# Optimization experiments

Measured on AMD Instinct MI355X. Metric: run time of the kernel, lower is better.

The kernel has to match this reference:

```python
import jax, jax.numpy as jnp
import numpy as np
from jax import lax

NF = 64
KS = 3
PAD = 1
TOPK = 2
DG = 8          # deformable_groups
N = KS * KS     # 9 sampling points


def conv3x3(x, w, b):
    y = lax.conv_general_dilated(x, w, (1, 1), 'SAME',
                                 dimension_numbers=('NCHW', 'OIHW', 'NCHW'))
    return y + b[None, :, None, None]


def lrelu(x):
    return jnp.where(x >= 0, x, 0.1 * x)


def dsp_sample(x, feat, w_om, b_om):
    """Modulated deformable sampling (DSP_sep2): returns the N bilinearly
    sampled, mask-modulated taps per pixel, shape (B, C, N, H, W)."""
    B, C, H, W = x.shape
    Cg = C // DG
    om = conv3x3(feat, w_om, b_om)              # (B, 3*DG*N, H, W)
    o1, o2, m = jnp.split(om, 3, axis=1)
    off_y = o1.reshape(B, DG, N, H, W)
    off_x = o2.reshape(B, DG, N, H, W)
    mask = jax.nn.sigmoid(m).reshape(B, DG, 1, N, H * W)
    kk = (jnp.arange(KS) - PAD).astype(jnp.float32)
    kdy = jnp.repeat(kk, KS)                    # (N,) kernel row offsets
    kdx = jnp.tile(kk, KS)                      # (N,) kernel col offsets
    ii = jnp.arange(H, dtype=jnp.float32)
    jj = jnp.arange(W, dtype=jnp.float32)
    ys = ii[None, None, None, :, None] + kdy[None, None, :, None, None] + off_y
    xs = jj[None, None, None, None, :] + kdx[None, None, :, None, None] + off_x
    y0 = jnp.floor(ys)
    x0 = jnp.floor(xs)
    xf = x.reshape(B, DG, Cg, H * W)
    out = jnp.zeros((B, DG, Cg, N, H * W), x.dtype)
    # bilinear interpolation with zero padding outside the image
    for dy in (0.0, 1.0):
        for dx in (0.0, 1.0):
            yi = y0 + dy
            xi = x0 + dx
            wgt = (1.0 - jnp.abs(ys - yi)) * (1.0 - jnp.abs(xs - xi))
            valid = (yi >= 0) & (yi <= H - 1) & (xi >= 0) & (xi <= W - 1)
            lin = (jnp.clip(yi, 0, H - 1) * W + jnp.clip(xi, 0, W - 1)).astype(jnp.int32)
            g = jnp.take_along_axis(xf[:, :, :, None, :],
                                    lin.reshape(B, DG, 1, N, H * W), axis=-1)
            out = out + g * jnp.where(valid, wgt, 0.0).reshape(B, DG, 1, N, H * W)
    return (out * mask).reshape(B, C, N, H, W)


def setup_inputs() -> dict:
    key = jax.random.key(0)
    ks = jax.random.split(key, 9)
    B, C, H, W = 2, NF, 192, 192

    def rn(k, s, sc=1.0):
        return jax.random.normal(k, s, jnp.float32) * sc

    return {
        'query': rn(ks[0], (B, C, H, W)),
        'key':   rn(ks[1], (B, C, H, W)),
        'value': rn(ks[2], (B, C, H, W)),
        'w1': rn(ks[3], (C, 2 * C, 3, 3), 0.05), 'b1': rn(ks[4], (C,), 0.05),
        'w2': rn(ks[5], (C, C, 3, 3), 0.05),     'b2': rn(ks[6], (C,), 0.05),
        'w_om': rn(ks[7], (3 * DG * N, C, 3, 3), 0.01),
        'b_om': rn(ks[8], (3 * DG * N,), 0.01),
    }


def reference(query, key, value, w1, b1, w2, b2, w_om, b_om):
    B, C, H, W = query.shape
    HW = H * W
    feat = lrelu(conv3x3(jnp.concatenate([query, key], axis=1), w1, b1))
    feat = lrelu(conv3x3(feat, w2, b2))
    # deformable sampled keys: (B, C, N, H, W) -> (B, HW, N, C)
    key_off = dsp_sample(key, feat, w_om, b_om).transpose(0, 3, 4, 2, 1).reshape(B, HW, N, C)
    q = query.reshape(B, C, HW).transpose(0, 2, 1)            # (B, HW, C)
    rel = jnp.einsum('bpnc,bpc->bpn', key_off, q)             # relevance scores
    topv, topi = lax.top_k(rel, TOPK)                         # (B, HW, TOPK)
    corr = jax.nn.softmax(topv, axis=-1)
    val_off = dsp_sample(value, feat, w_om, b_om).transpose(0, 3, 4, 2, 1).reshape(B, HW, N, C)
    k_sel = jnp.take_along_axis(key_off, topi[..., None], axis=2)  # (B, HW, TOPK, C)
    v_sel = jnp.take_along_axis(val_off, topi[..., None], axis=2)
    k_upd = jnp.einsum('bptc,bpt->bpc', k_sel, corr)
    v_out = jnp.einsum('bptc,bpt->bpc', v_sel, corr).transpose(0, 2, 1)  # (B, C, HW)
    weight = jnp.einsum('bpc,bpc->bp', q, k_upd)              # (B, HW)
    return (weight, v_out)
```

## Files before the change

kernel.cpp:

```cpp
#include <hip/hip_runtime.h>
#include <math.h>

#define H_  192
#define W_  192
#define HW_ (192 * 192)
#define B_  2
#define C_  64

typedef __attribute__((ext_vector_type(8))) short short8;
typedef __attribute__((ext_vector_type(4))) short short4v;
typedef __attribute__((ext_vector_type(4))) float float4v;
typedef _Float16 __attribute__((ext_vector_type(8))) half8;

union hbits { _Float16 f; short s; };
__device__ __forceinline__ void split2(float x, short& h, short& l) {
    _Float16 hf = (_Float16)x;
    float r = (x - (float)hf) * 4096.f;
    _Float16 lf = (_Float16)r;
    hbits u;
    u.f = hf; h = u.s;
    u.f = lf; l = u.s;
}

__device__ __forceinline__ float bilin_dot(const float* __restrict__ pl,
                                           float ys, float xs, int c4,
                                           float4v q4) {
    float y0 = floorf(ys), x0 = floorf(xs);
    float fy = ys - y0, fx = xs - x0;
    int iy = (int)y0, ix = (int)x0;
    float acc = 0.f;
    #pragma unroll
    for (int dy = 0; dy < 2; ++dy) {
        #pragma unroll
        for (int dx = 0; dx < 2; ++dx) {
            int yy = iy + dy, xx = ix + dx;
            float wgt = (dy ? fy : 1.f - fy) * (dx ? fx : 1.f - fx);
            bool valid = (yy >= 0) && (yy < H_) && (xx >= 0) && (xx < W_);
            int yc = min(max(yy, 0), H_ - 1);
            int xc = min(max(xx, 0), W_ - 1);
            const float4v v = *(const float4v*)(pl + (size_t)(yc * W_ + xc) * 64 + c4);
            float d = v[0] * q4[0] + v[1] * q4[1] + v[2] * q4[2] + v[3] * q4[3];
            acc += valid ? wgt * d : 0.f;
        }
    }
    return acc;
}
__device__ __forceinline__ float4v bilin_v4(const float* __restrict__ pl,
                                            float ys, float xs, int c4) {
    float y0 = floorf(ys), x0 = floorf(xs);
    float fy = ys - y0, fx = xs - x0;
    int iy = (int)y0, ix = (int)x0;
    float4v acc;
    acc[0] = acc[1] = acc[2] = acc[3] = 0.f;
    #pragma unroll
    for (int dy = 0; dy < 2; ++dy) {
        #pragma unroll
        for (int dx = 0; dx < 2; ++dx) {
            int yy = iy + dy, xx = ix + dx;
            float wgt = (dy ? fy : 1.f - fy) * (dx ? fx : 1.f - fx);
            bool valid = (yy >= 0) && (yy < H_) && (xx >= 0) && (xx < W_);
            float wz = valid ? wgt : 0.f;
            int yc = min(max(yy, 0), H_ - 1);
            int xc = min(max(xx, 0), W_ - 1);
            const float4v v = *(const float4v*)(pl + (size_t)(yc * W_ + xc) * 64 + c4);
            #pragma unroll
            for (int r = 0; r < 4; ++r) acc[r] += wz * v[r];
        }
    }
    return acc;
}

__global__ __launch_bounds__(256) void prep_w_k(
    const float* __restrict__ w1, const float* __restrict__ w2,
    const float* __restrict__ wom,
    short* __restrict__ pw1, short* __restrict__ pw2, short* __restrict__ pwom)
{
    int idx = blockIdx.x * 256 + threadIdx.x;
    int arr;
    if (idx < 144 * 512) { arr = 0; }
    else if (idx < (144 + 72) * 512) { arr = 1; idx -= 144 * 512; }
    else if (idx < (144 + 72 + 252) * 512) { arr = 2; idx -= (144 + 72) * 512; }
    else return;
    int frag = idx >> 9, within = idx & 511;
    int lane = within >> 3, j = within & 7;
    int KS   = (arr == 0) ? 4 : 2;
    int mt   = frag / (9 * KS);
    int rem  = frag % (9 * KS);
    int kk   = rem / KS;
    int s    = rem % KS;
    int co   = mt * 16 + (lane & 15);
    int c    = s * 32 + (lane >> 4) * 8 + j;
    float v = 0.f;
    if (arr == 0)      v = w1[(co * 128 + c) * 9 + kk];
    else if (arr == 1) v = w2[(co * 64 + c) * 9 + kk];
    else if (co < 216) v = wom[(co * 64 + c) * 9 + kk];
    short h, l;
    split2(v, h, l);
    short* dst = (arr == 0) ? pw1 : (arr == 1) ? pw2 : pwom;
    size_t base = (size_t)frag * 1024 + lane * 8 + j;
    dst[base]       = h;
    dst[base + 512] = l;
}

__global__ __launch_bounds__(256) void nchw_to_nhwc(
    const float* __restrict__ key, const float* __restrict__ value,
    float* __restrict__ kT, float* __restrict__ vT)
{
    __shared__ float sm[64][65];
    const int tid = threadIdx.x;
    const int p0  = blockIdx.x * 64;
    const int b   = blockIdx.y;
    const float* src = blockIdx.z ? value : key;
    float*       dst = blockIdx.z ? vT    : kT;
    const int pp = tid & 63;
    const int r0 = tid >> 6;
    #pragma unroll
    for (int c = r0; c < 64; c += 4)
        sm[c][pp] = src[(size_t)(b * 64 + c) * HW_ + p0 + pp];
    __syncthreads();
    const int cc = tid & 63;
    #pragma unroll
    for (int pw = r0; pw < 64; pw += 4)
        dst[((size_t)b * HW_ + p0 + pw) * 64 + cc] = sm[cc][pw];
}

template<int CIN, int MT, bool LRELU, int OUTMODE, bool FROMF32>
__global__ __launch_bounds__(256) void conv_mfma(
    const void* __restrict__ in0v, const void* __restrict__ in1v,
    const short* __restrict__ pw, const float* __restrict__ bias,
    void* __restrict__ outv)
{
    constexpr int KS   = CIN / 32;
    constexpr int MTW  = MT / 2;
    constexpr int LSTR = 72;
    __shared__ __align__(16) short smem[66 * LSTR];

    const int tid  = threadIdx.x;
    const int lane = tid & 63;
    const int w    = tid >> 6;
    const int wh   = w & 1;
    const int wn   = w >> 1;
    const int quad = lane >> 4;
    const int nn   = lane & 15;

    const int flat = blockIdx.x;
    const int xcd  = flat & 7;
    const int cc_  = flat >> 3;
    const int b    = xcd >> 2;
    const int r4   = xcd & 3;
    const int i    = r4 * 48 + cc_ / 3;
    const int j0   = (cc_ % 3) * 64;
    const int mt0  = wh * MTW;

    constexpr float CSC = 1.f / 4096.f;

    float4v accM[MTW][2];
    #pragma unroll
    for (int m = 0; m < MTW; ++m)
        #pragma unroll
        for (int t = 0; t < 2; ++t)
            #pragma unroll
            for (int r = 0; r < 4; ++r) accM[m][t][r] = 0.f;

    float4v zvec;
    zvec[0] = zvec[1] = zvec[2] = zvec[3] = 0.f;

    for (int ky = 0; ky < 3; ++ky) {
        const int row = i + ky - 1;
        const bool rowok = (row >= 0) && (row < H_);
        for (int s = 0; s < KS; ++s) {
            __syncthreads();
            if (FROMF32) {
                const float* src = (s < KS / 2) ? (const float*)in0v
                                                : (const float*)in1v;
                const int cbase = (s & (KS / 2 - 1)) * 32;
                for (int idx = tid; idx < 32 * 66; idx += 256) {
                    int ci = idx / 66, px = idx - ci * 66;
                    int col = j0 - 1 + px;
                    float v = 0.f;
                    if (rowok && col >= 0 && col < W_)
                        v = src[(size_t)(b * 64 + cbase + ci) * HW_ + row * W_ + col];
                    short h, l;
                    split2(v, h, l);
                    smem[px * LSTR + ci]      = h;
                    smem[px * LSTR + 32 + ci] = l;
                }
            } else {
                const short* src = (const short*)in0v
                                 + (size_t)b * HW_ * (2 * CIN);
                for (int idx = tid; idx < 66 * 16; idx += 256) {
                    int px = idx >> 4, r = idx & 15;
                    int limb = r >> 3, dq = r & 7;
                    int col = j0 - 1 + px;
                    unsigned long long v = 0;
                    if (rowok && col >= 0 && col < W_)
                        v = *(const unsigned long long*)(src
                              + (size_t)(row * W_ + col) * (2 * CIN)
                              + limb * CIN + s * 32 + dq * 4);
                    *(unsigned long long*)(&smem[px * LSTR + limb * 32 + dq * 4]) = v;
                }
            }
            __syncthreads();

            #pragma unroll
            for (int kx = 0; kx < 3; ++kx) {
                const int kk = ky * 3 + kx;
                half8 bh[2], bl[2];
                #pragma unroll
                for (int t2 = 0; t2 < 2; ++t2) {
                    const int t = wn * 2 + t2;
                    const short* bp = &smem[(t * 16 + nn + kx) * LSTR + quad * 8];
                    bh[t2] = *(const half8*)bp;
                    bl[t2] = *(const half8*)(bp + 32);
                }
                #pragma unroll
                for (int m = 0; m < MTW; ++m) {
                    const short* ap = pw
                        + ((size_t)(((mt0 + m) * 9 + kk) * KS + s)) * 1024
                        + lane * 8;
                    half8 ah = *(const half8*)ap;
                    half8 al = *(const half8*)(ap + 512);
                    float4v t0, t1;
                    accM[m][0] = __builtin_amdgcn_mfma_f32_16x16x32_f16(ah, bh[0], accM[m][0], 0, 0, 0);
                    t0         = __builtin_amdgcn_mfma_f32_16x16x32_f16(ah, bl[0], zvec,       0, 0, 0);
                    accM[m][1] = __builtin_amdgcn_mfma_f32_16x16x32_f16(ah, bh[1], accM[m][1], 0, 0, 0);
                    t1         = __builtin_amdgcn_mfma_f32_16x16x32_f16(ah, bl[1], zvec,       0, 0, 0);
                    t0         = __builtin_amdgcn_mfma_f32_16x16x32_f16(al, bh[0], t0,         0, 0, 0);
                    t1         = __builtin_amdgcn_mfma_f32_16x16x32_f16(al, bh[1], t1,         0, 0, 0);
                    #pragma unroll
                    for (int r = 0; r < 4; ++r) {
                        accM[m][0][r] += t0[r] * CSC;
                        accM[m][1][r] += t1[r] * CSC;
                    }
                }
            }
        }
    }

    #pragma unroll
    for (int m = 0; m < MTW; ++m) {
        const int co0 = (mt0 + m) * 16 + quad * 4;
        #pragma unroll
        for (int t2 = 0; t2 < 2; ++t2) {
            const int t = wn * 2 + t2;
            const int p = i * W_ + j0 + t * 16 + nn;
            if (OUTMODE == 0) {
                short* feat = (short*)outv;
                short4v hv, lv;
                #pragma unroll
                for (int r = 0; r < 4; ++r) {
                    float x = accM[m][t2][r] + bias[co0 + r];
                    if (LRELU) x = (x >= 0.f) ? x : 0.1f * x;
                    short h, l;
                    split2(x, h, l);
                    hv[r] = h; lv[r] = l;
                }
                short* dp = feat + ((size_t)b * HW_ + p) * 128 + co0;
                *(short4v*)dp        = hv;
                *(short4v*)(dp + 64) = lv;
            } else {
                if (co0 < 216) {
                    float* om = (float*)outv;
                    float4v v;
                    #pragma unroll
                    for (int r = 0; r < 4; ++r)
                        v[r] = accM[m][t2][r] + bias[co0 + r];
                    *(float4v*)(om + ((size_t)b * HW_ + p) * 216 + co0) = v;
                }
            }
        }
    }
}

__global__ __launch_bounds__(256) void sampler_k(
    const float* __restrict__ query, const float* __restrict__ kT,
    const float* __restrict__ vT, const float* __restrict__ om,
    float* __restrict__ out_w, float* __restrict__ out_v)
{
    __shared__ float sq[16 * 68];
    const int tid  = threadIdx.x;
    const int bb   = blockIdx.x;
    const int b    = bb / 2304;
    const int pblk = (bb - b * 2304) * 16;

    #pragma unroll
    for (int k = 0; k < 4; ++k) {
        int idx = tid + k * 256;
        int c   = idx >> 4;
        int px  = idx & 15;
        sq[px * 68 + c] = query[(size_t)(b * 64 + c) * HW_ + pblk + px];
    }
    __syncthreads();

    const int lane   = tid & 63;
    const int w      = tid >> 6;
    const int px_sub = lane >> 4;
    const int cl     = lane & 15;
    const int c4     = cl * 4;
    const int g      = cl >> 1;
    const int p      = pblk + w * 4 + px_sub;
    const int i      = p / W_;
    const int j      = p - i * W_;

    const float4v q4 = *(const float4v*)&sq[(w * 4 + px_sub) * 68 + c4];

    const float* omb = om + ((size_t)b * HW_ + p) * 216;
    float offy[9], offx[9], mk[9];
    #pragma unroll
    for (int n = 0; n < 9; ++n) {
        offy[n] = omb[g * 9 + n];
        offx[n] = omb[72 + g * 9 + n];
        float mv = omb[144 + g * 9 + n];
        mk[n] = 1.f / (1.f + expf(-mv));
    }

    const float* kpl = kT + (size_t)b * HW_ * 64;
    float rel[9];
    #pragma unroll
    for (int n = 0; n < 9; ++n) {
        float ys = (float)i + (float)(n / 3 - 1) + offy[n];
        float xs = (float)j + (float)(n % 3 - 1) + offx[n];
        float d = bilin_dot(kpl, ys, xs, c4, q4) * mk[n];
        #pragma unroll
        for (int off = 1; off < 16; off <<= 1)
            d += __shfl_xor(d, off, 64);
        rel[n] = d;
    }

    int n0 = 0; float v0 = rel[0];
    #pragma unroll
    for (int n = 1; n < 9; ++n) { if (rel[n] > v0) { v0 = rel[n]; n0 = n; } }
    int n1 = -1; float v1 = -1e30f;
    #pragma unroll
    for (int n = 0; n < 9; ++n) { if (n != n0 && rel[n] > v1) { v1 = rel[n]; n1 = n; } }

    float e1  = expf(v1 - v0);
    float inv = 1.f / (1.f + e1);
    float c0 = inv, c1 = e1 * inv;

    if (cl == 0) out_w[(size_t)b * HW_ + p] = c0 * v0 + c1 * v1;

    float oy0 = 0, ox0 = 0, m0 = 0, oy1 = 0, ox1 = 0, m1 = 0;
    #pragma unroll
    for (int n = 0; n < 9; ++n) {
        if (n == n0) { oy0 = offy[n]; ox0 = offx[n]; m0 = mk[n]; }
        if (n == n1) { oy1 = offy[n]; ox1 = offx[n]; m1 = mk[n]; }
    }

    const float* vpl = vT + (size_t)b * HW_ * 64;
    float ys0 = (float)i + (float)(n0 / 3 - 1) + oy0;
    float xs0 = (float)j + (float)(n0 % 3 - 1) + ox0;
    float ys1 = (float)i + (float)(n1 / 3 - 1) + oy1;
    float xs1 = (float)j + (float)(n1 % 3 - 1) + ox1;
    float4v vv0 = bilin_v4(vpl, ys0, xs0, c4);
    float4v vv1 = bilin_v4(vpl, ys1, xs1, c4);
    float w0 = c0 * m0, w1s = c1 * m1;
    #pragma unroll
    for (int r = 0; r < 4; ++r)
        out_v[(size_t)(b * C_ + c4 + r) * HW_ + p] = w0 * vv0[r] + w1s * vv1[r];
}

extern "C" void kernel_launch(void* const* d_in, const int* in_sizes, int n_in,
                              void* d_out, int out_size, void* d_ws, size_t ws_size,
                              hipStream_t stream)
{
    const float* query = (const float*)d_in[0];
    const float* key   = (const float*)d_in[1];
    const float* value = (const float*)d_in[2];
    const float* w1    = (const float*)d_in[3];
    const float* b1    = (const float*)d_in[4];
    const float* w2    = (const float*)d_in[5];
    const float* b2    = (const float*)d_in[6];
    const float* wom   = (const float*)d_in[7];
    const float* bom   = (const float*)d_in[8];
    float* out = (float*)d_out;

    char* ws = (char*)d_ws;
    short* f1  = (short*)(ws);
    float* om  = (float*)(ws);
    short* f2  = (short*)(ws + 63700992);
    float* kT  = (float*)(ws + 63700992);
    float* vT  = (float*)(ws + 82575360);
    short* pwom= (short*)(ws + 92012544);
    short* pw1 = (short*)(ws + 92786688);
    short* pw2 = (short*)(ws + 93229056);

    prep_w_k<<<936, 256, 0, stream>>>(w1, w2, wom, pw1, pw2, pwom);

    conv_mfma<128, 4,  true,  0, true ><<<1152, 256, 0, stream>>>(query, key, pw1, b1, (void*)f1);
    conv_mfma<64,  4,  true,  0, false><<<1152, 256, 0, stream>>>(f1, nullptr, pw2, b2, (void*)f2);
    conv_mfma<64,  14, false, 1, false><<<1152, 256, 0, stream>>>(f2, nullptr, pwom, bom, (void*)om);

    nchw_to_nhwc<<<dim3(576, B_, 2), 256, 0, stream>>>(key, value, kT, vT);

    float* out_w = out;
    float* out_v = out + (size_t)B_ * HW_;
    sampler_k<<<(B_ * HW_) / 16, 256, 0, stream>>>(query, kT, vT, om, out_w, out_v);
}
```

Before: 429.8 us.

## Stage all input channels per kernel row in LDS with XOR swizzle

The conv kernel now loads every input-channel slice for a kernel row into shared memory in one pass, instead of one 32-channel slice at a time. This cuts the number of barriers and load phases from KS per row to one. For the fp32-input variant it adds an XOR swizzle on the LDS column index to reduce bank conflicts, and the hi/lo-split variant loads contiguous 8-byte chunks. The cost is a much larger LDS footprint (up to about 37KB), which may lower occupancy.

```diff
diff --git a/kernel.cpp b/kernel.cpp
--- a/kernel.cpp
+++ b/kernel.cpp
@@ -132,7 +132,7 @@
 {
     constexpr int KS   = CIN / 32;
     constexpr int MTW  = MT / 2;
-    constexpr int LSTR = 72;
+    constexpr int LSTR = FROMF32 ? 280 : 136;
     __shared__ __align__(16) short smem[66 * LSTR];
 
     const int tid  = threadIdx.x;
@@ -168,50 +168,58 @@
     for (int ky = 0; ky < 3; ++ky) {
         const int row = i + ky - 1;
         const bool rowok = (row >= 0) && (row < H_);
-        for (int s = 0; s < KS; ++s) {
-            __syncthreads();
-            if (FROMF32) {
-                const float* src = (s < KS / 2) ? (const float*)in0v
-                                                : (const float*)in1v;
-                const int cbase = (s & (KS / 2 - 1)) * 32;
-                for (int idx = tid; idx < 32 * 66; idx += 256) {
-                    int ci = idx / 66, px = idx - ci * 66;
-                    int col = j0 - 1 + px;
-                    float v = 0.f;
-                    if (rowok && col >= 0 && col < W_)
-                        v = src[(size_t)(b * 64 + cbase + ci) * HW_ + row * W_ + col];
-                    short h, l;
-                    split2(v, h, l);
-                    smem[px * LSTR + ci]      = h;
-                    smem[px * LSTR + 32 + ci] = l;
+        __syncthreads();
+        if (FROMF32) {
+            for (int idx = tid; idx < 128 * 66; idx += 256) {
+                int ci = idx / 66, px = idx - ci * 66;
+                int col = j0 - 1 + px;
+                float v = 0.f;
+                if (rowok && col >= 0 && col < W_) {
+                    const float* src = (ci < 64) ? (const float*)in0v
+                                                 : (const float*)in1v;
+                    v = src[(size_t)(b * 64 + (ci & 63)) * HW_ + row * W_ + col];
                 }
-            } else {
-                const short* src = (const short*)in0v
-                                 + (size_t)b * HW_ * (2 * CIN);
-                for (int idx = tid; idx < 66 * 16; idx += 256) {
-                    int px = idx >> 4, r = idx & 15;
-                    int limb = r >> 3, dq = r & 7;
-                    int col = j0 - 1 + px;
-                    unsigned long long v = 0;
-                    if (rowok && col >= 0 && col < W_)
-                        v = *(const unsigned long long*)(src
-                              + (size_t)(row * W_ + col) * (2 * CIN)
-                              + limb * CIN + s * 32 + dq * 4);
-                    *(unsigned long long*)(&smem[px * LSTR + limb * 32 + dq * 4]) = v;
-                }
+                short h, l;
+                split2(v, h, l);
+                int s   = ci >> 5;
+                int c5  = ci & 31;
+                int msk = ((px >> 3) & 7) << 3;
+                short* rp = &smem[px * LSTR];
+                rp[(s * 64 + c5) ^ msk]      = h;
+                rp[(s * 64 + 32 + c5) ^ msk] = l;
             }
-            __syncthreads();
-
+        } else {
+            const short* srcb = (const short*)in0v + (size_t)b * HW_ * (2 * CIN);
+            for (int idx = tid; idx < 66 * (CIN / 2); idx += 256) {
+                int px = idx / (CIN / 2), r = idx - px * (CIN / 2);
+                int col = j0 - 1 + px;
+                unsigned long long v = 0;
+                if (rowok && col >= 0 && col < W_)
+                    v = *(const unsigned long long*)(srcb
+                          + (size_t)(row * W_ + col) * (2 * CIN) + r * 4);
+                *(unsigned long long*)(&smem[px * LSTR + r * 4]) = v;
+            }
+        }
+        __syncthreads();
+
+        #pragma unroll
+        for (int kx = 0; kx < 3; ++kx) {
+            const int kk = ky * 3 + kx;
             #pragma unroll
-            for (int kx = 0; kx < 3; ++kx) {
-                const int kk = ky * 3 + kx;
+            for (int s = 0; s < KS; ++s) {
                 half8 bh[2], bl[2];
                 #pragma unroll
                 for (int t2 = 0; t2 < 2; ++t2) {
-                    const int t = wn * 2 + t2;
-                    const short* bp = &smem[(t * 16 + nn + kx) * LSTR + quad * 8];
-                    bh[t2] = *(const half8*)bp;
-                    bl[t2] = *(const half8*)(bp + 32);
+                    const int rr = (wn * 2 + t2) * 16 + nn + kx;
+                    const short* rp = &smem[rr * LSTR];
+                    if (FROMF32) {
+                        const int msk = ((rr >> 3) & 7) << 3;
+                        bh[t2] = *(const half8*)&rp[(s * 64 + quad * 8) ^ msk];
+                        bl[t2] = *(const half8*)&rp[(s * 64 + 32 + quad * 8) ^ msk];
+                    } else {
+                        bh[t2] = *(const half8*)&rp[s * 32 + quad * 8];
+                        bl[t2] = *(const half8*)&rp[CIN + s * 32 + quad * 8];
+                    }
                 }
                 #pragma unroll
                 for (int m = 0; m < MTW; ++m) {
```

Measured after the change: 438.1 us. No clear change (+1.9%).

## Pre-pad inputs into split-fp16 NHWC and read conv operands directly from global

Applied to the files above, without the earlier changes.

Adds a pack kernel that converts query/key into a zero-padded NHWC hi/lo fp16 buffer, and makes the intermediate feature maps padded with zeroed borders. The conv kernels then drop the LDS staging, the barriers and the per-pixel boundary checks, and load MFMA B operands straight from global memory. In exchange there are extra kernels and padded buffers, and the same input pixels are loaded repeatedly from global/L2 rather than once per block into shared memory. The workspace offsets are also rearranged, so buffers that share memory need checking.

```diff
diff --git a/kernel.cpp b/kernel.cpp
--- a/kernel.cpp
+++ b/kernel.cpp
@@ -6,6 +6,7 @@
 #define HW_ (192 * 192)
 #define B_  2
 #define C_  64
+#define PW_ 194
 
 typedef __attribute__((ext_vector_type(8))) short short8;
 typedef __attribute__((ext_vector_type(4))) short short4v;
@@ -102,6 +103,49 @@
     dst[base + 512] = l;
 }
 
+__global__ __launch_bounds__(256) void pack_qk(
+    const float* __restrict__ q, const float* __restrict__ k,
+    short* __restrict__ qk2)
+{
+    const int prow = blockIdx.x;
+    const int b    = blockIdx.y;
+    const int row  = prow - 1;
+    const bool rok = (row >= 0) && (row < H_);
+    short* dst = qk2 + ((size_t)(b * PW_ + prow) * PW_) * 256;
+    for (int idx = threadIdx.x; idx < 128 * PW_; idx += 256) {
+        int ci = idx / PW_, pcol = idx - ci * PW_;
+        int col = pcol - 1;
+        float v = 0.f;
+        if (rok && col >= 0 && col < W_) {
+            const float* src = (ci < 64) ? q : k;
+            v = src[(size_t)(b * 64 + (ci & 63)) * HW_ + row * W_ + col];
+        }
+        short h, l;
+        split2(v, h, l);
+        dst[(size_t)pcol * 256 + ci]       = h;
+        dst[(size_t)pcol * 256 + 128 + ci] = l;
+    }
+}
+
+__global__ __launch_bounds__(256) void zero_borders(
+    short* __restrict__ f1p, short* __restrict__ f2p)
+{
+    const int prow = blockIdx.x;
+    const int b    = blockIdx.y;
+    short* dst = (blockIdx.z ? f2p : f1p) + ((size_t)(b * PW_ + prow) * PW_) * 128;
+    if (prow == 0 || prow == PW_ - 1) {
+        for (int idx = threadIdx.x; idx < PW_ * 128; idx += 256) dst[idx] = 0;
+    } else {
+        for (int idx = threadIdx.x; idx < 256; idx += 256) {
+            dst[idx] = 0;
+            dst[(size_t)(PW_ - 1) * 128 + idx - 128 * (idx >> 7)] = 0;
+        }
+        int t = threadIdx.x;
+        if (t < 128) dst[t] = 0;
+        else dst[(size_t)(PW_ - 1) * 128 + (t - 128)] = 0;
+    }
+}
+
 __global__ __launch_bounds__(256) void nchw_to_nhwc(
     const float* __restrict__ key, const float* __restrict__ value,
     float* __restrict__ kT, float* __restrict__ vT)
@@ -124,16 +168,13 @@
         dst[((size_t)b * HW_ + p0 + pw) * 64 + cc] = sm[cc][pw];
 }
 
-template<int CIN, int MT, bool LRELU, int OUTMODE, bool FROMF32>
-__global__ __launch_bounds__(256) void conv_mfma(
-    const void* __restrict__ in0v, const void* __restrict__ in1v,
-    const short* __restrict__ pw, const float* __restrict__ bias,
-    void* __restrict__ outv)
-{
-    constexpr int KS   = CIN / 32;
-    constexpr int MTW  = MT / 2;
-    constexpr int LSTR = 72;
-    __shared__ __align__(16) short smem[66 * LSTR];
+template<int CIN, int MT, bool LRELU, int OUTMODE>
+__global__ __launch_bounds__(256) void conv_direct(
+    const short* __restrict__ in, const short* __restrict__ pw,
+    const float* __restrict__ bias, void* __restrict__ outv)
+{
+    constexpr int KS  = CIN / 32;
+    constexpr int MTW = MT / 2;
 
     const int tid  = threadIdx.x;
     const int lane = tid & 63;
@@ -166,52 +207,20 @@
     zvec[0] = zvec[1] = zvec[2] = zvec[3] = 0.f;
 
     for (int ky = 0; ky < 3; ++ky) {
-        const int row = i + ky - 1;
-        const bool rowok = (row >= 0) && (row < H_);
-        for (int s = 0; s < KS; ++s) {
-            __syncthreads();
-            if (FROMF32) {
-                const float* src = (s < KS / 2) ? (const float*)in0v
-                                                : (const float*)in1v;
-                const int cbase = (s & (KS / 2 - 1)) * 32;
-                for (int idx = tid; idx < 32 * 66; idx += 256) {
-                    int ci = idx / 66, px = idx - ci * 66;
-                    int col = j0 - 1 + px;
-                    float v = 0.f;
-                    if (rowok && col >= 0 && col < W_)
-                        v = src[(size_t)(b * 64 + cbase + ci) * HW_ + row * W_ + col];
-                    short h, l;
-                    split2(v, h, l);
-                    smem[px * LSTR + ci]      = h;
-                    smem[px * LSTR + 32 + ci] = l;
-                }
-            } else {
-                const short* src = (const short*)in0v
-                                 + (size_t)b * HW_ * (2 * CIN);
-                for (int idx = tid; idx < 66 * 16; idx += 256) {
-                    int px = idx >> 4, r = idx & 15;
-                    int limb = r >> 3, dq = r & 7;
-                    int col = j0 - 1 + px;
-                    unsigned long long v = 0;
-                    if (rowok && col >= 0 && col < W_)
-                        v = *(const unsigned long long*)(src
-                              + (size_t)(row * W_ + col) * (2 * CIN)
-                              + limb * CIN + s * 32 + dq * 4);
-                    *(unsigned long long*)(&smem[px * LSTR + limb * 32 + dq * 4]) = v;
-                }
-            }
-            __syncthreads();
-
+        const short* rowp = in + ((size_t)(b * PW_ + (i + ky)) * PW_) * (2 * CIN);
+        #pragma unroll
+        for (int kx = 0; kx < 3; ++kx) {
+            const int kk = ky * 3 + kx;
             #pragma unroll
-            for (int kx = 0; kx < 3; ++kx) {
-                const int kk = ky * 3 + kx;
+            for (int s = 0; s < KS; ++s) {
                 half8 bh[2], bl[2];
                 #pragma unroll
                 for (int t2 = 0; t2 < 2; ++t2) {
-                    const int t = wn * 2 + t2;
-                    const short* bp = &smem[(t * 16 + nn + kx) * LSTR + quad * 8];
+                    const int pcol = j0 + kx + (wn * 2 + t2) * 16 + nn;
+                    const short* bp = rowp + (size_t)pcol * (2 * CIN)
+                                    + s * 32 + quad * 8;
                     bh[t2] = *(const half8*)bp;
-                    bl[t2] = *(const half8*)(bp + 32);
+                    bl[t2] = *(const half8*)(bp + CIN);
                 }
                 #pragma unroll
                 for (int m = 0; m < MTW; ++m) {
@@ -243,8 +252,9 @@
         #pragma unroll
         for (int t2 = 0; t2 < 2; ++t2) {
             const int t = wn * 2 + t2;
-            const int p = i * W_ + j0 + t * 16 + nn;
             if (OUTMODE == 0) {
+                const size_t pp = ((size_t)(b * PW_ + i + 1) * PW_
+                                   + (j0 + t * 16 + nn + 1)) * 128;
                 short* feat = (short*)outv;
                 short4v hv, lv;
                 #pragma unroll
@@ -255,11 +265,11 @@
                     split2(x, h, l);
                     hv[r] = h; lv[r] = l;
                 }
-                short* dp = feat + ((size_t)b * HW_ + p) * 128 + co0;
-                *(short4v*)dp        = hv;
-                *(short4v*)(dp + 64) = lv;
+                *(short4v*)(feat + pp + co0)      = hv;
+                *(short4v*)(feat + pp + 64 + co0) = lv;
             } else {
                 if (co0 < 216) {
+                    const int p = i * W_ + j0 + t * 16 + nn;
                     float* om = (float*)outv;
                     float4v v;
                     #pragma unroll
@@ -376,20 +386,23 @@
     float* out = (float*)d_out;
 
     char* ws = (char*)d_ws;
-    short* f1  = (short*)(ws);
-    float* om  = (float*)(ws);
-    short* f2  = (short*)(ws + 63700992);
-    float* kT  = (float*)(ws + 63700992);
-    float* vT  = (float*)(ws + 82575360);
-    short* pwom= (short*)(ws + 92012544);
-    short* pw1 = (short*)(ws + 92786688);
-    short* pw2 = (short*)(ws + 93229056);
-
+    float* om   = (float*)(ws);
+    short* f1p  = (short*)(ws);
+    short* qk2  = (short*)(ws + 19269632);
+    short* pw1  = (short*)(ws + 57808896);
+    short* pw2  = (short*)(ws + 58103808);
+    short* f2p  = (short*)(ws + 63700992);
+    short* pwom = (short*)(ws + 82970624);
+    float* kT   = (float*)(ws + 63700992);
+    float* vT   = (float*)(ws + 82575360);
+
+    zero_borders<<<dim3(PW_, B_, 2), 256, 0, stream>>>(f1p, f2p);
+    pack_qk<<<dim3(PW_, B_), 256, 0, stream>>>(query, key, qk2);
     prep_w_k<<<936, 256, 0, stream>>>(w1, w2, wom, pw1, pw2, pwom);
 
-    conv_mfma<128, 4,  true,  0, true ><<<1152, 256, 0, stream>>>(query, key, pw1, b1, (void*)f1);
-    conv_mfma<64,  4,  true,  0, false><<<1152, 256, 0, stream>>>(f1, nullptr, pw2, b2, (void*)f2);
-    conv_mfma<64,  14, false, 1, false><<<1152, 256, 0, stream>>>(f2, nullptr, pwom, bom, (void*)om);
+    conv_direct<128, 4,  true,  0><<<1152, 256, 0, stream>>>(qk2, pw1, b1, (void*)f1p);
+    conv_direct<64,  4,  true,  0><<<1152, 256, 0, stream>>>(f1p, pw2, b2, (void*)f2p);
+    conv_direct<64,  14, false, 1><<<1152, 256, 0, stream>>>(f2p, pwom, bom, (void*)om);
 
     nchw_to_nhwc<<<dim3(576, B_, 2), 256, 0, stream>>>(key, value, kT, vT);
 
```

New measurement: 668.3 us. 1.55x slower.

## Stage offset/mask tile in LDS, precompute sigmoid, remap blocks by XCD

Applied to the files above, without the earlier changes.

The conv epilogue now applies the sigmoid to the mask channels before storing, so the sampler no longer computes it per lane. The sampler stages each block's 16x216 offset/mask tile into shared memory with coalesced float4 loads, replacing scattered per-lane global reads. Block indices are also remapped so that each XCD works on a contiguous band of rows in one batch, which should improve L2 locality for the gathered key/value rows. The cost is extra LDS use per block and a remap that assumes the grid size matches this exact layout.

```diff
diff --git a/kernel.cpp b/kernel.cpp
--- a/kernel.cpp
+++ b/kernel.cpp
@@ -265,6 +265,11 @@
                     #pragma unroll
                     for (int r = 0; r < 4; ++r)
                         v[r] = accM[m][t2][r] + bias[co0 + r];
+                    if (co0 >= 144) {
+                        #pragma unroll
+                        for (int r = 0; r < 4; ++r)
+                            v[r] = 1.f / (1.f + expf(-v[r]));
+                    }
                     *(float4v*)(om + ((size_t)b * HW_ + p) * 216 + co0) = v;
                 }
             }
@@ -278,10 +283,15 @@
     float* __restrict__ out_w, float* __restrict__ out_v)
 {
     __shared__ float sq[16 * 68];
+    __shared__ float som[16 * 220];
     const int tid  = threadIdx.x;
-    const int bb   = blockIdx.x;
-    const int b    = bb / 2304;
-    const int pblk = (bb - b * 2304) * 16;
+    const int flat = blockIdx.x;
+    const int xcd  = flat & 7;
+    const int cc_  = flat >> 3;
+    const int b    = xcd >> 2;
+    const int r4   = xcd & 3;
+    const int row  = r4 * 48 + cc_ / 12;
+    const int pblk = row * W_ + (cc_ % 12) * 16;
 
     #pragma unroll
     for (int k = 0; k < 4; ++k) {
@@ -289,6 +299,16 @@
         int c   = idx >> 4;
         int px  = idx & 15;
         sq[px * 68 + c] = query[(size_t)(b * 64 + c) * HW_ + pblk + px];
+    }
+    {
+        const float4v* omp = (const float4v*)(om + ((size_t)b * HW_ + pblk) * 216);
+        for (int u = tid; u < 864; u += 256) {
+            float4v v = omp[u];
+            int px  = u / 54;
+            int c4i = (u - px * 54) * 4;
+            float* d = &som[px * 220 + c4i];
+            d[0] = v[0]; d[1] = v[1]; d[2] = v[2]; d[3] = v[3];
+        }
     }
     __syncthreads();
 
@@ -298,20 +318,20 @@
     const int cl     = lane & 15;
     const int c4     = cl * 4;
     const int g      = cl >> 1;
-    const int p      = pblk + w * 4 + px_sub;
+    const int pxl    = w * 4 + px_sub;
+    const int p      = pblk + pxl;
     const int i      = p / W_;
     const int j      = p - i * W_;
 
-    const float4v q4 = *(const float4v*)&sq[(w * 4 + px_sub) * 68 + c4];
-
-    const float* omb = om + ((size_t)b * HW_ + p) * 216;
+    const float4v q4 = *(const float4v*)&sq[pxl * 68 + c4];
+
+    const float* somp = &som[pxl * 220];
     float offy[9], offx[9], mk[9];
     #pragma unroll
     for (int n = 0; n < 9; ++n) {
-        offy[n] = omb[g * 9 + n];
-        offx[n] = omb[72 + g * 9 + n];
-        float mv = omb[144 + g * 9 + n];
-        mk[n] = 1.f / (1.f + expf(-mv));
+        offy[n] = somp[g * 9 + n];
+        offx[n] = somp[72 + g * 9 + n];
+        mk[n]   = somp[144 + g * 9 + n];
     }
 
     const float* kpl = kT + (size_t)b * HW_ * 64;
```

New measurement: 424.3 us. No clear change (-1.3%).
